# Performance work log

Measured on AMD Instinct MI355X. Metric: run time of the kernel, lower is better.

Reference implementation:

```python
import jax, jax.numpy as jnp
import numpy as np

B = 8192
E = 1024  # embedding_size
P = 512   # projection_size
TEMPERATURE = 0.1
NEG_INF = -9e15
EPS = 1e-8


def setup_inputs() -> dict:
    key = jax.random.key(0)
    kx, kw, kb = jax.random.split(key, 3)
    x = jax.random.normal(kx, (B, 2 * E), dtype=jnp.float32)
    lim = 1.0 / np.sqrt(E)
    # torch nn.Linear default init: uniform(-1/sqrt(in), 1/sqrt(in))
    w = jax.random.uniform(kw, (E, P), jnp.float32, -lim, lim)
    b = jax.random.uniform(kb, (P,), jnp.float32, -lim, lim)
    return {"x": x, "w": w, "b": b}


def reference(x, w, b):
    e = x.shape[1] // 2
    # NOTE: source applies codon_projection to BOTH halves (aminoacid_projection unused)
    z_codon = jax.nn.relu(x[:, :e]) @ w + b          # [B, P]
    z_amino = jax.nn.relu(x[:, e:]) @ w + b          # [B, P]
    z = jnp.concatenate([z_codon, z_amino], axis=1)  # [B, 2P]

    # cosine similarity via normalize + GEMM instead of O(B^2*D) broadcast
    norm = jnp.maximum(jnp.linalg.norm(z, axis=-1, keepdims=True), EPS)
    zn = z / norm
    cos_sim = zn @ zn.T                              # [B, B]

    n = cos_sim.shape[0]
    idx = jnp.arange(n)
    # mask self-similarity BEFORE temperature division (matches source order)
    cos_sim = jnp.where(idx[:, None] == idx[None, :], NEG_INF, cos_sim)
    cos_sim = cos_sim / TEMPERATURE

    # pos_mask = eye rolled by B//2 along dim 0: pos[i] = cos_sim[i, (i - B//2) % B]
    pos = cos_sim[idx, (idx - n // 2) % n]
    nll = -pos + jax.nn.logsumexp(cos_sim, axis=-1)
    return nll.mean()
```

## Files before the change

### kernel.cpp

```cpp
#include <hip/hip_runtime.h>
#include <hip/hip_bf16.h>
#include <stdint.h>


typedef __attribute__((ext_vector_type(4))) float f32x4;
typedef __attribute__((ext_vector_type(4))) int i32x4;
typedef __attribute__((ext_vector_type(8))) int i32x8;

__device__ __forceinline__ unsigned int enc4(float v) {
  unsigned int s = (__float_as_uint(v) >> 28) & 8u;
  float a = fabsf(v);
  unsigned int m;
  if (a < 0.25f) m = 0u;
  else if (a < 0.75f) m = 1u;
  else if (a < 1.25f) m = 2u;
  else if (a < 1.75f) m = 3u;
  else if (a < 2.5f)  m = 4u;
  else if (a < 3.5f)  m = 5u;
  else if (a < 5.0f)  m = 6u;
  else m = 7u;
  return s | m;
}

__global__ __launch_bounds__(256) void wtr_kernel(
    const float* __restrict__ w, unsigned char* __restrict__ wt8,
    float* __restrict__ sumexp, float* __restrict__ out) {
  __shared__ unsigned char lt[64][68];
  int b = blockIdx.x, t = threadIdx.x;
  int gt = b * 256 + t;
  if (gt < 8192) sumexp[gt] = 0.f;
  if (gt == 0) out[0] = 0.f;
  int k0 = (b >> 3) * 64, n0 = (b & 7) * 64;
  int r = t >> 4, c = t & 15;
#pragma unroll
  for (int i = 0; i < 4; ++i) {
    int kl = i * 16 + r;
    float4 v = *(const float4*)&w[(size_t)(k0 + kl) * 512 + n0 + c * 4];
    int q = __builtin_amdgcn_cvt_pk_fp8_f32(v.x * 64.f, v.y * 64.f, 0, false);
    q = __builtin_amdgcn_cvt_pk_fp8_f32(v.z * 64.f, v.w * 64.f, q, true);
    *(int*)&lt[kl][c * 4] = q;
  }
  __syncthreads();
  int nl = t >> 2, ks = t & 3;
  union { unsigned char b8[16]; i32x4 v4; } u;
#pragma unroll
  for (int j = 0; j < 16; ++j) u.b8[j] = lt[ks * 16 + j][nl];
  *(i32x4*)&wt8[(size_t)(n0 + nl) * 1024 + k0 + ks * 16] = u.v4;
}

__global__ __launch_bounds__(512) void gemm1qn_kernel(
    const float* __restrict__ x, const unsigned char* __restrict__ wt8,
    const float* __restrict__ bias, unsigned char* __restrict__ zn4) {
  __shared__ unsigned char smem[16384] __attribute__((aligned(16)));
  int i0 = blockIdx.x * 64;
  int tid = threadIdx.x, L = tid & 63, w = tid >> 6;
  int l4 = L & 15, q = L >> 4;

  int ra = tid >> 3, kq = tid & 7;
  int Aoff = (kq >> 1) * 2048 + ((((ra * 2) ^ ((ra >> 2) & 7)) ^ (kq & 1))) * 16;
  const float* xq = x + (size_t)(i0 + ra) * 1024 + kq * 16;

  auto writeA = [&](int buf, const float4* xv) {
    int pk[4];
#pragma unroll
    for (int j = 0; j < 4; ++j) {
      int p = __builtin_amdgcn_cvt_pk_fp8_f32(fmaxf(xv[j].x, 0.f) * 16.f,
                                              fmaxf(xv[j].y, 0.f) * 16.f, 0, false);
      p = __builtin_amdgcn_cvt_pk_fp8_f32(fmaxf(xv[j].z, 0.f) * 16.f,
                                          fmaxf(xv[j].w, 0.f) * 16.f, p, true);
      pk[j] = p;
    }
    *(i32x4*)(smem + buf * 8192 + Aoff) = (i32x4){pk[0], pk[1], pk[2], pk[3]};
  };

  int pAo[4];
#pragma unroll
  for (int mt = 0; mt < 4; ++mt) {
    int r = mt * 16 + l4;
    pAo[mt] = ((r * 2) ^ ((r >> 2) & 7)) * 16;
  }

  const unsigned char* bp[4];
#pragma unroll
  for (int nt = 0; nt < 4; ++nt) {
    int r = w * 64 + nt * 16 + l4;
    bp[nt] = wt8 + (size_t)r * 1024 + q * 32;
  }

  f32x4 acc[4][4];
#pragma unroll
  for (int a = 0; a < 4; ++a)
#pragma unroll
    for (int bq = 0; bq < 4; ++bq) acc[a][bq] = (f32x4)0.f;

  float4 xv[4];
#pragma unroll
  for (int j = 0; j < 4; ++j) xv[j] = *(const float4*)(xq + j * 4);
  writeA(0, xv);
  i32x4 b0[4][2], b1[4][2];
#pragma unroll
  for (int nt = 0; nt < 4; ++nt) {
    b0[nt][0] = *(const i32x4*)(bp[nt]);
    b0[nt][1] = *(const i32x4*)(bp[nt] + 16);
  }
  __syncthreads();

  auto step = [&](int s, i32x4 (&bu)[4][2], i32x4 (&bl)[4][2]) {
    if (s < 7) {
#pragma unroll
      for (int j = 0; j < 4; ++j)
        xv[j] = *(const float4*)(xq + (s + 1) * 128 + j * 4);
#pragma unroll
      for (int nt = 0; nt < 4; ++nt) {
        bl[nt][0] = *(const i32x4*)(bp[nt] + (s + 1) * 128);
        bl[nt][1] = *(const i32x4*)(bp[nt] + (s + 1) * 128 + 16);
      }
    }
    const unsigned char* Ab = smem + (s & 1) * 8192 + q * 2048;
    i32x8 afr[4];
#pragma unroll
    for (int mt = 0; mt < 4; ++mt) {
      i32x4 lo = *(const i32x4*)(Ab + pAo[mt]);
      i32x4 hi = *(const i32x4*)(Ab + (pAo[mt] ^ 16));
      afr[mt] = (i32x8){lo.x, lo.y, lo.z, lo.w, hi.x, hi.y, hi.z, hi.w};
    }
#pragma unroll
    for (int nt = 0; nt < 4; ++nt) {
      i32x8 bfr = (i32x8){bu[nt][0].x, bu[nt][0].y, bu[nt][0].z, bu[nt][0].w,
                          bu[nt][1].x, bu[nt][1].y, bu[nt][1].z, bu[nt][1].w};
#pragma unroll
      for (int mt = 0; mt < 4; ++mt)
        acc[mt][nt] = __builtin_amdgcn_mfma_scale_f32_16x16x128_f8f6f4(
            afr[mt], bfr, acc[mt][nt], 0, 0,
            0, 0x7F7F7F7F, 0, 0x7F7F7F7F);
    }
    if (s < 7) writeA((s + 1) & 1, xv);
    __syncthreads();
  };
  step(0, b0, b1); step(1, b1, b0); step(2, b0, b1); step(3, b1, b0);
  step(4, b0, b1); step(5, b1, b0); step(6, b0, b1); step(7, b1, b0);

  const float SC = 1.0f / 1024.0f;
  float bn[4];
#pragma unroll
  for (int nt = 0; nt < 4; ++nt) bn[nt] = bias[w * 64 + nt * 16 + l4];
  float ssp[4][4];
#pragma unroll
  for (int mt = 0; mt < 4; ++mt)
#pragma unroll
    for (int r = 0; r < 4; ++r) ssp[mt][r] = 0.f;
#pragma unroll
  for (int mt = 0; mt < 4; ++mt)
#pragma unroll
    for (int nt = 0; nt < 4; ++nt)
#pragma unroll
      for (int r = 0; r < 4; ++r) {
        float zv = acc[mt][nt][r] * SC + bn[nt];
        acc[mt][nt][r] = zv;
        ssp[mt][r] += zv * zv;
      }
#pragma unroll
  for (int mt = 0; mt < 4; ++mt)
#pragma unroll
    for (int r = 0; r < 4; ++r) {
      float v = ssp[mt][r];
      v += __shfl_xor(v, 1); v += __shfl_xor(v, 2);
      v += __shfl_xor(v, 4); v += __shfl_xor(v, 8);
      ssp[mt][r] = v;
    }
  float* ssbuf = (float*)smem;
  if (l4 == 0) {
#pragma unroll
    for (int mt = 0; mt < 4; ++mt)
#pragma unroll
      for (int r = 0; r < 4; ++r)
        ssbuf[(mt * 16 + q * 4 + r) * 8 + w] = ssp[mt][r];
  }
  __syncthreads();
  float* invbuf = (float*)(smem + 2048);
  if (tid < 32) {
    float tot = 0.f;
#pragma unroll
    for (int j = 0; j < 8; ++j)
      tot += ssbuf[(2 * tid) * 8 + j] + ssbuf[(2 * tid + 1) * 8 + j];
    invbuf[tid] = 32.f / fmaxf(sqrtf(tot), 1e-8f);
  }
  __syncthreads();
#pragma unroll
  for (int mt = 0; mt < 4; ++mt)
#pragma unroll
    for (int r = 0; r < 4; ++r) {
      int zr = mt * 16 + q * 4 + r;
      float inv = invbuf[zr >> 1];
      int zg = i0 + zr;
      size_t base = (size_t)(zg >> 1) * 512 + (size_t)(zg & 1) * 256;
#pragma unroll
      for (int nt = 0; nt < 4; ++nt) {
        unsigned int n = enc4(acc[mt][nt][r] * inv);
        unsigned int hi = (unsigned int)__shfl_xor((int)n, 1);
        if (!(l4 & 1)) {
          int col = w * 64 + nt * 16 + l4;
          zn4[base + (col >> 1)] = (unsigned char)(n | (hi << 4));
        }
      }
    }
}

__global__ __launch_bounds__(256, 3) void gemm2_kernel(
    const unsigned char* __restrict__ zn4,
    float* __restrict__ sumexp, float* __restrict__ pos) {
  __shared__ unsigned char As[8192] __attribute__((aligned(16)));
  __shared__ unsigned char Bs[8192] __attribute__((aligned(16)));
  int g = (blockIdx.x & 7) * 260 + (blockIdx.x >> 3);
  int SI = 0, rem = g;
#pragma unroll 1
  for (SI = 0; SI < 8; ++SI) {
    int rowcnt = 36 + (7 - SI) * 64;
    if (rem < rowcnt) break;
    rem -= rowcnt;
  }
  int bi, bj;
  if (rem < 36) {
    int ti = 0;
    while (rem >= 8 - ti) { rem -= 8 - ti; ++ti; }
    bi = SI * 8 + ti;
    bj = bi + rem;
  } else {
    rem -= 36;
    int SJ = SI + 1 + (rem >> 6);
    int l = rem & 63;
    bi = SI * 8 + (l >> 3);
    bj = SJ * 8 + (l & 7);
  }
  bool diag = (bi == bj);
  int i0 = bi * 128, j0 = bj * 128;

  int tid = threadIdx.x, L = tid & 63, w = tid >> 6;
  int wm = w >> 1, wn = w & 1;
  int l4 = L & 15, q = L >> 4;

  int strow = tid >> 2;
  int sq = (tid & 3) ^ ((tid >> 3) & 3);
  const unsigned char* Ag  = zn4 + (size_t)(i0 + strow) * 512 + sq * 16;
  const unsigned char* Ag2 = Ag + 64 * 512;
  const unsigned char* Bg  = zn4 + (size_t)(j0 + strow) * 512 + sq * 16;
  const unsigned char* Bg2 = Bg + 64 * 512;
  int ldb = (tid & ~63) * 16;

  int pA[4], pB[4];
#pragma unroll
  for (int mt = 0; mt < 4; ++mt) {
    int r = wm * 64 + mt * 16 + l4;
    pA[mt] = r * 64 + ((q ^ ((r >> 1) & 3)) << 4);
  }
#pragma unroll
  for (int nt = 0; nt < 4; ++nt) {
    int r = wn * 64 + nt * 16 + l4;
    pB[nt] = r * 64 + ((q ^ ((r >> 1) & 3)) << 4);
  }

  f32x4 acc[4][4];
#pragma unroll
  for (int a = 0; a < 4; ++a)
#pragma unroll
    for (int bq = 0; bq < 4; ++bq) acc[a][bq] = (f32x4)0.f;

  const unsigned char* Bsrc = diag ? (const unsigned char*)As : (const unsigned char*)Bs;

#pragma unroll 1
  for (int koff = 0; koff < 512; koff += 64) {
    __syncthreads();
    __builtin_amdgcn_global_load_lds(
        (const __attribute__((address_space(1))) void*)(Ag + koff),
        (__attribute__((address_space(3))) void*)(As + ldb), 16, 0, 0);
    __builtin_amdgcn_global_load_lds(
        (const __attribute__((address_space(1))) void*)(Ag2 + koff),
        (__attribute__((address_space(3))) void*)(As + 4096 + ldb), 16, 0, 0);
    if (!diag) {
      __builtin_amdgcn_global_load_lds(
          (const __attribute__((address_space(1))) void*)(Bg + koff),
          (__attribute__((address_space(3))) void*)(Bs + ldb), 16, 0, 0);
      __builtin_amdgcn_global_load_lds(
          (const __attribute__((address_space(1))) void*)(Bg2 + koff),
          (__attribute__((address_space(3))) void*)(Bs + 4096 + ldb), 16, 0, 0);
    }
    __syncthreads();
    i32x4 a4[4];
#pragma unroll
    for (int mt = 0; mt < 4; ++mt) a4[mt] = *(const i32x4*)(As + pA[mt]);
#pragma unroll
    for (int nt = 0; nt < 4; ++nt) {
      i32x4 b4 = *(const i32x4*)(Bsrc + pB[nt]);
      i32x8 bfr = (i32x8){b4.x, b4.y, b4.z, b4.w, b4.x, b4.y, b4.z, b4.w};
#pragma unroll
      for (int mt = 0; mt < 4; ++mt) {
        i32x8 afr = (i32x8){a4[mt].x, a4[mt].y, a4[mt].z, a4[mt].w,
                            a4[mt].x, a4[mt].y, a4[mt].z, a4[mt].w};
        acc[mt][nt] = __builtin_amdgcn_mfma_scale_f32_16x16x128_f8f6f4(
            afr, bfr, acc[mt][nt], 4, 4,
            0, 0x7F7F7F7F, 0, 0x7F7F7F7F);
      }
    }
  }

  const float SC = 10.0f / 1024.0f;
  float rs[4][4];
  float cs[4] = {0.f, 0.f, 0.f, 0.f};
#pragma unroll
  for (int mt = 0; mt < 4; ++mt)
#pragma unroll
    for (int r = 0; r < 4; ++r) rs[mt][r] = 0.f;
  int ib = i0 + wm * 64 + (q << 2);
  int jb = j0 + wn * 64 + l4;
#pragma unroll
  for (int mt = 0; mt < 4; ++mt)
#pragma unroll
    for (int nt = 0; nt < 4; ++nt) {
      int j = jb + nt * 16;
#pragma unroll
      for (int r = 0; r < 4; ++r) {
        int i = ib + mt * 16 + r;
        float s = acc[mt][nt][r] * SC;
        if (j == (i ^ 4096)) { pos[i] = s; pos[j] = s; }
        float e = (i == j) ? 0.f : __expf(s);
        rs[mt][r] += e;
        if (!diag) cs[nt] += e;
      }
    }
#pragma unroll
  for (int mt = 0; mt < 4; ++mt)
#pragma unroll
    for (int r = 0; r < 4; ++r) {
      float v = rs[mt][r];
      v += __shfl_xor(v, 1); v += __shfl_xor(v, 2);
      v += __shfl_xor(v, 4); v += __shfl_xor(v, 8);
      rs[mt][r] = v;
    }
  int sel = l4;
  float myv = rs[0][0];
#pragma unroll
  for (int mt = 0; mt < 4; ++mt)
#pragma unroll
    for (int r = 0; r < 4; ++r)
      if (sel == mt * 4 + r) myv = rs[mt][r];
  int rowi = i0 + wm * 64 + (sel >> 2) * 16 + (q << 2) + (sel & 3);
  atomicAdd(&sumexp[rowi], myv);
  if (!diag) {
#pragma unroll
    for (int nt = 0; nt < 4; ++nt) {
      float v = cs[nt];
      v += __shfl_xor(v, 16); v += __shfl_xor(v, 32);
      if (q == 0) atomicAdd(&sumexp[jb + nt * 16], v);
    }
  }
}

__global__ __launch_bounds__(512) void finalize_kernel(
    const float* __restrict__ sumexp, const float* __restrict__ pos,
    float* __restrict__ out) {
  int t = threadIdx.x;
  int i = blockIdx.x * 512 + t;
  float s = logf(sumexp[i]) - pos[i];
#pragma unroll
  for (int off = 1; off < 64; off <<= 1) s += __shfl_xor(s, off);
  __shared__ float red[8];
  if ((t & 63) == 0) red[t >> 6] = s;
  __syncthreads();
  if (t == 0) {
    float tot = 0.f;
    for (int k2 = 0; k2 < 8; ++k2) tot += red[k2];
    atomicAdd(out, tot * (1.0f / 8192.0f));
  }
}

extern "C" void kernel_launch(void* const* d_in, const int* in_sizes, int n_in,
                              void* d_out, int out_size, void* d_ws, size_t ws_size,
                              hipStream_t stream) {
  const float* x = (const float*)d_in[0];
  const float* w = (const float*)d_in[1];
  const float* b = (const float*)d_in[2];
  float* out = (float*)d_out;
  char* ws = (char*)d_ws;
  unsigned char* wt8 = (unsigned char*)(ws);
  unsigned char* zn4 = (unsigned char*)(ws + 68157440);
  float* sumexp      = (float*)(ws + 84934656);
  float* pos         = (float*)(ws + 84967424);

  wtr_kernel<<<128, 256, 0, stream>>>(w, wt8, sumexp, out);
  gemm1qn_kernel<<<256, 512, 0, stream>>>(x, wt8, b, zn4);
  gemm2_kernel<<<2080, 256, 0, stream>>>(zn4, sumexp, pos);
  finalize_kernel<<<16, 512, 0, stream>>>(sumexp, pos, out);
}
```

Before: 153.4 us.

## Stagger K-loop start per block and prefetch x two stages ahead

In the projection GEMM, each block now walks the K chunks in a rotated order based on its block index, so blocks do not all hit the same columns of x and wt8 at once. The x loads are prefetched two steps ahead using a second register buffer, and __syncthreads is replaced by an explicit lgkmcnt wait plus s_barrier with scheduling fences, so global loads in flight are not drained at each barrier. The cosine-similarity GEMM loop also rotates its K offset per block. This costs extra registers for the second x buffer and depends on the order-independent K accumulation giving the same result.

```diff
diff --git a/kernel.cpp b/kernel.cpp
--- a/kernel.cpp
+++ b/kernel.cpp
@@ -52,7 +52,8 @@
     const float* __restrict__ x, const unsigned char* __restrict__ wt8,
     const float* __restrict__ bias, unsigned char* __restrict__ zn4) {
   __shared__ unsigned char smem[16384] __attribute__((aligned(16)));
-  int i0 = blockIdx.x * 64;
+  int bid = blockIdx.x;
+  int i0 = bid * 64;
   int tid = threadIdx.x, L = tid & 63, w = tid >> 6;
   int l4 = L & 15, q = L >> 4;
 
@@ -93,28 +94,47 @@
 #pragma unroll
     for (int bq = 0; bq < 4; ++bq) acc[a][bq] = (f32x4)0.f;
 
-  float4 xv[4];
-#pragma unroll
-  for (int j = 0; j < 4; ++j) xv[j] = *(const float4*)(xq + j * 4);
-  writeA(0, xv);
+  auto ph = [&](int t) { return (t + bid) & 7; };
+
+  float4 xv0[4], xv1[4];
   i32x4 b0[4][2], b1[4][2];
-#pragma unroll
-  for (int nt = 0; nt < 4; ++nt) {
-    b0[nt][0] = *(const i32x4*)(bp[nt]);
-    b0[nt][1] = *(const i32x4*)(bp[nt] + 16);
-  }
-  __syncthreads();
-
-  auto step = [&](int s, i32x4 (&bu)[4][2], i32x4 (&bl)[4][2]) {
+
+  {
+    int p0 = ph(0);
+#pragma unroll
+    for (int j = 0; j < 4; ++j) xv0[j] = *(const float4*)(xq + p0 * 128 + j * 4);
+    writeA(0, xv0);
+    int p1 = ph(1), p2 = ph(2);
+#pragma unroll
+    for (int j = 0; j < 4; ++j) xv1[j] = *(const float4*)(xq + p1 * 128 + j * 4);
+#pragma unroll
+    for (int j = 0; j < 4; ++j) xv0[j] = *(const float4*)(xq + p2 * 128 + j * 4);
+#pragma unroll
+    for (int nt = 0; nt < 4; ++nt) {
+      b0[nt][0] = *(const i32x4*)(bp[nt] + p0 * 128);
+      b0[nt][1] = *(const i32x4*)(bp[nt] + p0 * 128 + 16);
+    }
+    __builtin_amdgcn_sched_barrier(0);
+    asm volatile("s_waitcnt lgkmcnt(0)" ::: "memory");
+    __builtin_amdgcn_s_barrier();
+    __builtin_amdgcn_sched_barrier(0);
+  }
+
+  auto step = [&](int s, i32x4 (&bu)[4][2], i32x4 (&bl)[4][2],
+                  float4 (&xc)[4], float4 (&xl)[4]) {
     if (s < 7) {
+      int pn = ph(s + 1);
+#pragma unroll
+      for (int nt = 0; nt < 4; ++nt) {
+        bl[nt][0] = *(const i32x4*)(bp[nt] + pn * 128);
+        bl[nt][1] = *(const i32x4*)(bp[nt] + pn * 128 + 16);
+      }
+    }
+    if (s < 6) {
+      int pn2 = ph(s + 2);
 #pragma unroll
       for (int j = 0; j < 4; ++j)
-        xv[j] = *(const float4*)(xq + (s + 1) * 128 + j * 4);
-#pragma unroll
-      for (int nt = 0; nt < 4; ++nt) {
-        bl[nt][0] = *(const i32x4*)(bp[nt] + (s + 1) * 128);
-        bl[nt][1] = *(const i32x4*)(bp[nt] + (s + 1) * 128 + 16);
-      }
+        xl[j] = *(const float4*)(xq + pn2 * 128 + j * 4);
     }
     const unsigned char* Ab = smem + (s & 1) * 8192 + q * 2048;
     i32x8 afr[4];
@@ -134,11 +154,16 @@
             afr[mt], bfr, acc[mt][nt], 0, 0,
             0, 0x7F7F7F7F, 0, 0x7F7F7F7F);
     }
-    if (s < 7) writeA((s + 1) & 1, xv);
-    __syncthreads();
+    if (s < 7) writeA((s + 1) & 1, xc);
+    __builtin_amdgcn_sched_barrier(0);
+    asm volatile("s_waitcnt lgkmcnt(0)" ::: "memory");
+    __builtin_amdgcn_s_barrier();
+    __builtin_amdgcn_sched_barrier(0);
   };
-  step(0, b0, b1); step(1, b1, b0); step(2, b0, b1); step(3, b1, b0);
-  step(4, b0, b1); step(5, b1, b0); step(6, b0, b1); step(7, b1, b0);
+  step(0, b0, b1, xv1, xv0); step(1, b1, b0, xv0, xv1);
+  step(2, b0, b1, xv1, xv0); step(3, b1, b0, xv0, xv1);
+  step(4, b0, b1, xv1, xv0); step(5, b1, b0, xv0, xv1);
+  step(6, b0, b1, xv1, xv0); step(7, b1, b0, xv0, xv1);
 
   const float SC = 1.0f / 1024.0f;
   float bn[4];
@@ -268,7 +293,8 @@
   const unsigned char* Bsrc = diag ? (const unsigned char*)As : (const unsigned char*)Bs;
 
 #pragma unroll 1
-  for (int koff = 0; koff < 512; koff += 64) {
+  for (int t = 0; t < 8; ++t) {
+    int koff = ((t + blockIdx.x) & 7) * 64;
     __syncthreads();
     __builtin_amdgcn_global_load_lds(
         (const __attribute__((address_space(1))) void*)(Ag + koff),
```

Result: no change. 155.0 us (+1.0%).
